# Optimization experiments

Measured on AMD Instinct MI355X. Metric: run time of the kernel, lower is better.

The kernel has to match this reference:

```python
import jax, jax.numpy as jnp
import numpy as np

B, S, D, H = 2, 2048, 1024, 16
DEPTH = D // H


def setup_inputs() -> dict:
    key = jax.random.key(0)
    ks = jax.random.split(key, 12)
    sc = 1.0 / np.sqrt(D)
    inp = {
        "q": jax.random.normal(ks[0], (B, S, D), jnp.float32),
        "v": jax.random.normal(ks[1], (B, S, D), jnp.float32),
        "k": jax.random.normal(ks[2], (B, S, D), jnp.float32),
        "mask": jnp.zeros((B, 1, S, S), jnp.float32),
        "wq_w": jax.random.normal(ks[3], (D, D), jnp.float32) * sc,
        "wq_b": jnp.zeros((D,), jnp.float32),
        "wk_w": jax.random.normal(ks[4], (D, D), jnp.float32) * sc,
        "wk_b": jnp.zeros((D,), jnp.float32),
        "wv_w": jax.random.normal(ks[5], (D, D), jnp.float32) * sc,
        "wv_b": jnp.zeros((D,), jnp.float32),
        "dense_w": jax.random.normal(ks[6], (D, D), jnp.float32) * sc,
        "dense_b": jnp.zeros((D,), jnp.float32),
    }
    return inp


def _split_heads(x):
    # (B, S, D) -> (B, H, S, depth)
    b, s, _ = x.shape
    return x.reshape(b, s, H, DEPTH).transpose(0, 2, 1, 3)


def reference(q, v, k, mask, wq_w, wq_b, wk_w, wk_b, wv_w, wv_b, dense_w, dense_b):
    batch_size = q.shape[0]
    # torch nn.Linear: x @ W.T + b
    qh = _split_heads(q @ wq_w.T + wq_b)
    kh = _split_heads(k @ wk_w.T + wk_b)
    vh = _split_heads(v @ wv_w.T + wv_b)
    temperature = jnp.asarray(DEPTH ** 0.5, qh.dtype)
    # scores: (B, H, Sq, Sk)
    qk = jnp.einsum("bhqd,bhkd->bhqk", qh, kh) / temperature
    qk = qk + mask * (-1e9)
    attention_weights = jax.nn.softmax(qk, axis=-1)
    out = jnp.einsum("bhqk,bhkd->bhqd", attention_weights, vh)
    out = out.transpose(0, 2, 1, 3).reshape(batch_size, -1, D)
    out = out @ dense_w.T + dense_b
    return (out, attention_weights)
```

## Files before the change

### kernel.cpp

```cpp
#include <hip/hip_runtime.h>
#include <cstdint>
#include <cstddef>

#define Bv   2
#define Sv   2048
#define Dv   1024
#define Hv   16
#define DEP  64
#define BHv  32
#define MROWS 4096

typedef float    f32x4 __attribute__((ext_vector_type(4)));
typedef float    f32x2 __attribute__((ext_vector_type(2)));
typedef _Float16 f16x8 __attribute__((ext_vector_type(8)));
typedef _Float16 f16x4 __attribute__((ext_vector_type(4)));
typedef _Float16 f16x2 __attribute__((ext_vector_type(2)));

__global__ __launch_bounds__(256) void convert_kernel(
    const float* __restrict__ q,  const float* __restrict__ k,  const float* __restrict__ v,
    const float* __restrict__ wq, const float* __restrict__ wk, const float* __restrict__ wv,
    const float* __restrict__ wd, const float* __restrict__ mask,
    _Float16* __restrict__ qx, _Float16* __restrict__ kx, _Float16* __restrict__ vx,
    _Float16* __restrict__ wqh, _Float16* __restrict__ wkh, _Float16* __restrict__ wvh,
    _Float16* __restrict__ wdh, _Float16* __restrict__ mlog)
{
    const size_t t = (size_t)blockIdx.x * 256 + threadIdx.x;
    {
        f32x4 m = *(const f32x4*)(mask + t * 4);
        const float sc = -1.442695040888963e9f;
        f32x4 s = { m.x * sc, m.y * sc, m.z * sc, m.w * sc };
        *(f16x4*)(mlog + t * 4) = __builtin_convertvector(s, f16x4);
    }
    {
        f32x2 a = *(const f32x2*)(q + t * 2);
        *(f16x2*)(qx + t * 2) = __builtin_convertvector(a, f16x2);
        f32x2 b = *(const f32x2*)(k + t * 2);
        *(f16x2*)(kx + t * 2) = __builtin_convertvector(b, f16x2);
        f32x2 c = *(const f32x2*)(v + t * 2);
        *(f16x2*)(vx + t * 2) = __builtin_convertvector(c, f16x2);
    }
    if (t < 524288) {
        f32x2 a = *(const f32x2*)(wq + t * 2);
        *(f16x2*)(wqh + t * 2) = __builtin_convertvector(a, f16x2);
        f32x2 b = *(const f32x2*)(wk + t * 2);
        *(f16x2*)(wkh + t * 2) = __builtin_convertvector(b, f16x2);
        f32x2 c = *(const f32x2*)(wv + t * 2);
        *(f16x2*)(wvh + t * 2) = __builtin_convertvector(c, f16x2);
        f32x2 d = *(const f32x2*)(wd + t * 2);
        *(f16x2*)(wdh + t * 2) = __builtin_convertvector(d, f16x2);
    }
}

#define LDT 40

__device__ __forceinline__ void gemm_core_128(
    const _Float16* __restrict__ A, const _Float16* __restrict__ W,
    int m0, int n0, _Float16* sA, _Float16* sW, f32x4 acc[4][4])
{
    const int tid  = threadIdx.x;
    const int lane = tid & 63, wave = tid >> 6;
    const int wm = (wave & 1) * 64, wn = (wave >> 1) * 64;
    const int fl = lane & 15, fq = lane >> 4;

    for (int k0 = 0; k0 < 1024; k0 += 32) {
        __syncthreads();
#pragma unroll
        for (int i = 0; i < 2; i++) {
            int s = tid + i * 256;
            int row = s >> 2, ch = s & 3;
            *(f16x8*)&sA[row * LDT + ch * 8] =
                *(const f16x8*)(A + (size_t)(m0 + row) * 1024 + k0 + ch * 8);
            *(f16x8*)&sW[row * LDT + ch * 8] =
                *(const f16x8*)(W + (size_t)(n0 + row) * 1024 + k0 + ch * 8);
        }
        __syncthreads();
        f16x8 af[4], wf[4];
#pragma unroll
        for (int i = 0; i < 4; i++)
            af[i] = *(const f16x8*)&sA[(wm + i * 16 + fl) * LDT + fq * 8];
#pragma unroll
        for (int j = 0; j < 4; j++)
            wf[j] = *(const f16x8*)&sW[(wn + j * 16 + fl) * LDT + fq * 8];
#pragma unroll
        for (int i = 0; i < 4; i++)
#pragma unroll
            for (int j = 0; j < 4; j++)
                acc[i][j] = __builtin_amdgcn_mfma_f32_16x16x32_f16(
                    af[i], wf[j], acc[i][j], 0, 0, 0);
    }
}

__global__ __launch_bounds__(256) void proj_gemm(
    const _Float16* __restrict__ qx, const _Float16* __restrict__ kx, const _Float16* __restrict__ vx,
    const _Float16* __restrict__ wqh, const _Float16* __restrict__ wkh, const _Float16* __restrict__ wvh,
    const float* __restrict__ bq, const float* __restrict__ bk, const float* __restrict__ bv,
    _Float16* __restrict__ qh, _Float16* __restrict__ kh, _Float16* __restrict__ vt)
{
    const _Float16* A; const _Float16* W; const float* bias; _Float16* outp; int transp;
    if (blockIdx.z == 0)      { A = qx; W = wqh; bias = bq; outp = qh; transp = 0; }
    else if (blockIdx.z == 1) { A = kx; W = wkh; bias = bk; outp = kh; transp = 0; }
    else                      { A = vx; W = wvh; bias = bv; outp = vt; transp = 1; }

    __shared__ _Float16 sA[128 * LDT];
    __shared__ _Float16 sW[128 * LDT];
    const int m0 = blockIdx.y * 128, n0 = blockIdx.x * 128;
    const int lane = threadIdx.x & 63, wave = threadIdx.x >> 6;
    const int wm = (wave & 1) * 64, wn = (wave >> 1) * 64;
    const int fl = lane & 15, fq = lane >> 4;

    f32x4 acc[4][4] = {};
    gemm_core_128(A, W, m0, n0, sA, sW, acc);

#pragma unroll
    for (int i = 0; i < 4; i++) {
#pragma unroll
        for (int j = 0; j < 4; j++) {
            int n = n0 + wn + j * 16 + fl;
            float bvv = bias[n];
            int h = n >> 6, d = n & 63;
#pragma unroll
            for (int r = 0; r < 4; r++) {
                int m = m0 + wm + i * 16 + fq * 4 + r;
                int b = m >> 11, s = m & 2047;
                float val = acc[i][j][r] + bvv;
                size_t addr;
                if (!transp) addr = (((size_t)(b * 16 + h) * 2048 + s) << 6) + d;
                else         addr = (((size_t)(b * 16 + h) * 64 + d) << 11) + s;
                outp[addr] = (_Float16)val;
            }
        }
    }
}

__global__ __launch_bounds__(256) void dense_gemm(
    const _Float16* __restrict__ A, const _Float16* __restrict__ W,
    const float* __restrict__ bias, float* __restrict__ outp)
{
    __shared__ _Float16 sA[128 * LDT];
    __shared__ _Float16 sW[128 * LDT];
    const int m0 = blockIdx.y * 128, n0 = blockIdx.x * 128;
    const int lane = threadIdx.x & 63, wave = threadIdx.x >> 6;
    const int wm = (wave & 1) * 64, wn = (wave >> 1) * 64;
    const int fl = lane & 15, fq = lane >> 4;

    f32x4 acc[4][4] = {};
    gemm_core_128(A, W, m0, n0, sA, sW, acc);

#pragma unroll
    for (int i = 0; i < 4; i++) {
#pragma unroll
        for (int j = 0; j < 4; j++) {
            int n = n0 + wn + j * 16 + fl;
            float bvv = bias[n];
#pragma unroll
            for (int r = 0; r < 4; r++) {
                int m = m0 + wm + i * 16 + fq * 4 + r;
                outp[(size_t)m * 1024 + n] = acc[i][j][r] + bvv;
            }
        }
    }
}

#define LK 72
#define LV 136
#define LP 136

__global__ __launch_bounds__(256) void attn_kernel(
    const _Float16* __restrict__ qh, const _Float16* __restrict__ kh,
    const _Float16* __restrict__ vt, const _Float16* __restrict__ mlog,
    float* __restrict__ attw, _Float16* __restrict__ ob)
{
    __shared__ _Float16 sK[128 * LK];
    __shared__ _Float16 sV[64 * LV];
    __shared__ _Float16 sP[4][16 * LP];

    const int tid = threadIdx.x, lane = tid & 63, wave = tid >> 6;
    const int bh = blockIdx.y;
    const int b  = bh >> 4;
    const int q0 = blockIdx.x * 64 + wave * 16;
    const int fl = lane & 15, fq = lane >> 4;
    const _Float16* Kb = kh + (size_t)bh * 2048 * 64;
    const _Float16* Vb = vt + (size_t)bh * 64 * 2048;
    const _Float16* Mb = mlog + ((size_t)b * 2048 + q0) * 2048;
    const float SC = 0.18033688011112042f;

    f16x8 qf[2];
    {
        const _Float16* Qb = qh + ((size_t)bh * 2048 + q0 + fl) * 64;
        qf[0] = *(const f16x8*)(Qb + fq * 8);
        qf[1] = *(const f16x8*)(Qb + 32 + fq * 8);
    }

    float lacc[4] = {0.f, 0.f, 0.f, 0.f};

    for (int kc = 0; kc < 16; kc++) {
        __syncthreads();
#pragma unroll
        for (int i = 0; i < 4; i++) {
            int s = tid + i * 256;
            int row = s >> 3, ch = s & 7;
            *(f16x8*)&sK[row * LK + ch * 8] =
                *(const f16x8*)(Kb + (size_t)(kc * 128 + row) * 64 + ch * 8);
        }
        __syncthreads();
#pragma unroll
        for (int nt = 0; nt < 8; nt++) {
            f16x8 kf0 = *(const f16x8*)&sK[(nt * 16 + fl) * LK + fq * 8];
            f16x8 kf1 = *(const f16x8*)&sK[(nt * 16 + fl) * LK + 32 + fq * 8];
            f32x4 sacc = {};
            sacc = __builtin_amdgcn_mfma_f32_16x16x32_f16(qf[0], kf0, sacc, 0, 0, 0);
            sacc = __builtin_amdgcn_mfma_f32_16x16x32_f16(qf[1], kf1, sacc, 0, 0, 0);
            int key = kc * 128 + nt * 16 + fl;
#pragma unroll
            for (int r = 0; r < 4; r++) {
                float mval = (float)Mb[(size_t)(fq * 4 + r) * 2048 + key];
                lacc[r] += exp2f(sacc[r] * SC + mval);
            }
        }
    }
#pragma unroll
    for (int r = 0; r < 4; r++) {
        float x = lacc[r];
        x += __shfl_xor(x, 1);
        x += __shfl_xor(x, 2);
        x += __shfl_xor(x, 4);
        x += __shfl_xor(x, 8);
        lacc[r] = 1.0f / x;
    }

    f32x4 oacc[4] = {};

    for (int kc = 0; kc < 16; kc++) {
        __syncthreads();
#pragma unroll
        for (int i = 0; i < 4; i++) {
            int s = tid + i * 256;
            int row = s >> 3, ch = s & 7;
            *(f16x8*)&sK[row * LK + ch * 8] =
                *(const f16x8*)(Kb + (size_t)(kc * 128 + row) * 64 + ch * 8);
        }
#pragma unroll
        for (int i = 0; i < 4; i++) {
            int s = tid + i * 256;
            int row = s >> 4, ch = s & 15;
            *(f16x8*)&sV[row * LV + ch * 8] =
                *(const f16x8*)(Vb + (size_t)row * 2048 + kc * 128 + ch * 8);
        }
        __syncthreads();
#pragma unroll
        for (int nt = 0; nt < 8; nt++) {
            f16x8 kf0 = *(const f16x8*)&sK[(nt * 16 + fl) * LK + fq * 8];
            f16x8 kf1 = *(const f16x8*)&sK[(nt * 16 + fl) * LK + 32 + fq * 8];
            f32x4 sacc = {};
            sacc = __builtin_amdgcn_mfma_f32_16x16x32_f16(qf[0], kf0, sacc, 0, 0, 0);
            sacc = __builtin_amdgcn_mfma_f32_16x16x32_f16(qf[1], kf1, sacc, 0, 0, 0);
            int key = kc * 128 + nt * 16 + fl;
#pragma unroll
            for (int r = 0; r < 4; r++) {
                float mval = (float)Mb[(size_t)(fq * 4 + r) * 2048 + key];
                float p = exp2f(sacc[r] * SC + mval) * lacc[r];
                attw[((size_t)bh * 2048 + q0 + fq * 4 + r) * 2048 + key] = p;
                sP[wave][(fq * 4 + r) * LP + nt * 16 + fl] = (_Float16)p;
            }
        }
        __syncthreads();
#pragma unroll
        for (int km = 0; km < 4; km++) {
            f16x8 pf = *(const f16x8*)&sP[wave][fl * LP + km * 32 + fq * 8];
#pragma unroll
            for (int dt = 0; dt < 4; dt++) {
                f16x8 vf = *(const f16x8*)&sV[(dt * 16 + fl) * LV + km * 32 + fq * 8];
                oacc[dt] = __builtin_amdgcn_mfma_f32_16x16x32_f16(pf, vf, oacc[dt], 0, 0, 0);
            }
        }
    }

    const int h = bh & 15;
#pragma unroll
    for (int dt = 0; dt < 4; dt++) {
#pragma unroll
        for (int r = 0; r < 4; r++) {
            int qrow = q0 + fq * 4 + r;
            ob[((size_t)(b * 2048 + qrow)) * 1024 + h * 64 + dt * 16 + fl] =
                (_Float16)oacc[dt][r];
        }
    }
}

extern "C" void kernel_launch(void* const* d_in, const int* in_sizes, int n_in,
                              void* d_out, int out_size, void* d_ws, size_t ws_size,
                              hipStream_t stream)
{
    const float* q       = (const float*)d_in[0];
    const float* v       = (const float*)d_in[1];
    const float* k       = (const float*)d_in[2];
    const float* mask    = (const float*)d_in[3];
    const float* wq_w    = (const float*)d_in[4];
    const float* wq_b    = (const float*)d_in[5];
    const float* wk_w    = (const float*)d_in[6];
    const float* wk_b    = (const float*)d_in[7];
    const float* wv_w    = (const float*)d_in[8];
    const float* wv_b    = (const float*)d_in[9];
    const float* dense_w = (const float*)d_in[10];
    const float* dense_b = (const float*)d_in[11];

    char* ws = (char*)d_ws;
    _Float16* qx   = (_Float16*)(ws + 0);
    _Float16* kx   = (_Float16*)(ws + 8388608);
    _Float16* vx   = (_Float16*)(ws + 16777216);
    _Float16* wqh  = (_Float16*)(ws + 25165824);
    _Float16* wkh  = (_Float16*)(ws + 27262976);
    _Float16* wvh  = (_Float16*)(ws + 29360128);
    _Float16* wdh  = (_Float16*)(ws + 31457280);
    _Float16* qhp  = (_Float16*)(ws + 33554432);
    _Float16* khp  = (_Float16*)(ws + 41943040);
    _Float16* vtp  = (_Float16*)(ws + 50331648);
    _Float16* obp  = (_Float16*)(ws + 58720256);
    _Float16* mlog = (_Float16*)(ws + 67108864);

    float* outp = (float*)d_out;
    float* attw = outp + (size_t)4194304;

    convert_kernel<<<8192, 256, 0, stream>>>(q, k, v, wq_w, wk_w, wv_w, dense_w,
                                             mask, qx, kx, vx, wqh, wkh, wvh, wdh, mlog);
    proj_gemm<<<dim3(8, 32, 3), 256, 0, stream>>>(qx, kx, vx, wqh, wkh, wvh,
                                                  wq_b, wk_b, wv_b, qhp, khp, vtp);
    attn_kernel<<<dim3(32, 32), 256, 0, stream>>>(qhp, khp, vtp, mlog, attw, obp);
    dense_gemm<<<dim3(8, 32), 256, 0, stream>>>(obp, wdh, dense_b, outp);
}
```

Baseline: 1.063 ms.

## Compute scores once per 16-row block, split keys across waves

The attention kernel is restructured so each block handles 16 query rows, and its four waves each take a quarter of the key range. Exponentiated scores are computed once and kept unnormalized in fp16 shared memory, instead of being recomputed in a second pass after the row sum is known. Row sums and partial P·V outputs are then reduced across waves through shared memory. The attention-weight output is written as coalesced vector stores, but those weights now come from fp16-rounded values, and K and V are read directly from global memory rather than staged in shared memory. The grid grows fourfold, and the large shared buffer (about 66 KB) may limit occupancy.

Measured after the change: 1.003 ms. -5.7%, faster.

```diff
diff --git a/kernel.cpp b/kernel.cpp
--- a/kernel.cpp
+++ b/kernel.cpp
@@ -161,129 +161,108 @@
     }
 }
 
-#define LK 72
-#define LV 136
-#define LP 136
+#define LPB 2056
 
 __global__ __launch_bounds__(256) void attn_kernel(
     const _Float16* __restrict__ qh, const _Float16* __restrict__ kh,
     const _Float16* __restrict__ vt, const _Float16* __restrict__ mlog,
     float* __restrict__ attw, _Float16* __restrict__ ob)
 {
-    __shared__ _Float16 sK[128 * LK];
-    __shared__ _Float16 sV[64 * LV];
-    __shared__ _Float16 sP[4][16 * LP];
-
-    const int tid = threadIdx.x, lane = tid & 63, wave = tid >> 6;
-    const int bh = blockIdx.y;
-    const int b  = bh >> 4;
-    const int q0 = blockIdx.x * 64 + wave * 16;
-    const int fl = lane & 15, fq = lane >> 4;
-    const _Float16* Kb = kh + (size_t)bh * 2048 * 64;
-    const _Float16* Vb = vt + (size_t)bh * 64 * 2048;
-    const _Float16* Mb = mlog + ((size_t)b * 2048 + q0) * 2048;
+    __shared__ _Float16 pbuf[16 * LPB];
+    __shared__ float    lred[4][16];
+
+    const int tid  = threadIdx.x, lane = tid & 63, wave = tid >> 6;
+    const int fl   = lane & 15,   fq   = lane >> 4;
+    const int bh   = blockIdx.y,  b    = bh >> 4, h = bh & 15;
+    const int q0   = blockIdx.x * 16;
+    const int kwb  = wave * 512;
     const float SC = 0.18033688011112042f;
 
-    f16x8 qf[2];
-    {
-        const _Float16* Qb = qh + ((size_t)bh * 2048 + q0 + fl) * 64;
-        qf[0] = *(const f16x8*)(Qb + fq * 8);
-        qf[1] = *(const f16x8*)(Qb + 32 + fq * 8);
-    }
-
-    float lacc[4] = {0.f, 0.f, 0.f, 0.f};
-
-    for (int kc = 0; kc < 16; kc++) {
-        __syncthreads();
-#pragma unroll
-        for (int i = 0; i < 4; i++) {
-            int s = tid + i * 256;
-            int row = s >> 3, ch = s & 7;
-            *(f16x8*)&sK[row * LK + ch * 8] =
-                *(const f16x8*)(Kb + (size_t)(kc * 128 + row) * 64 + ch * 8);
-        }
-        __syncthreads();
-#pragma unroll
-        for (int nt = 0; nt < 8; nt++) {
-            f16x8 kf0 = *(const f16x8*)&sK[(nt * 16 + fl) * LK + fq * 8];
-            f16x8 kf1 = *(const f16x8*)&sK[(nt * 16 + fl) * LK + 32 + fq * 8];
-            f32x4 sacc = {};
-            sacc = __builtin_amdgcn_mfma_f32_16x16x32_f16(qf[0], kf0, sacc, 0, 0, 0);
-            sacc = __builtin_amdgcn_mfma_f32_16x16x32_f16(qf[1], kf1, sacc, 0, 0, 0);
-            int key = kc * 128 + nt * 16 + fl;
-#pragma unroll
-            for (int r = 0; r < 4; r++) {
-                float mval = (float)Mb[(size_t)(fq * 4 + r) * 2048 + key];
-                lacc[r] += exp2f(sacc[r] * SC + mval);
-            }
-        }
-    }
-#pragma unroll
-    for (int r = 0; r < 4; r++) {
-        float x = lacc[r];
-        x += __shfl_xor(x, 1);
-        x += __shfl_xor(x, 2);
-        x += __shfl_xor(x, 4);
-        x += __shfl_xor(x, 8);
-        lacc[r] = 1.0f / x;
+    const _Float16* Kb   = kh   + (size_t)bh * 2048 * 64;
+    const _Float16* Vb   = vt   + (size_t)bh * 64 * 2048;
+    const _Float16* Mrow = mlog + ((size_t)b * 2048 + q0 + fl) * 2048 + kwb;
+
+    f16x8 qf0, qf1;
+    {
+        const _Float16* Qp = qh + ((size_t)bh * 2048 + q0 + fl) * 64;
+        qf0 = *(const f16x8*)(Qp + fq * 8);
+        qf1 = *(const f16x8*)(Qp + 32 + fq * 8);
+    }
+
+    float lacc = 0.f;
+#pragma unroll
+    for (int t = 0; t < 32; t++) {
+        const int key0 = kwb + t * 16;
+        const _Float16* Kp = Kb + (size_t)(key0 + fl) * 64 + fq * 8;
+        f16x8 kf0 = *(const f16x8*)Kp;
+        f16x8 kf1 = *(const f16x8*)(Kp + 32);
+        f16x4 mv  = *(const f16x4*)(Mrow + t * 16 + fq * 4);
+        f32x4 sacc = {};
+        sacc = __builtin_amdgcn_mfma_f32_16x16x32_f16(kf0, qf0, sacc, 0, 0, 0);
+        sacc = __builtin_amdgcn_mfma_f32_16x16x32_f16(kf1, qf1, sacc, 0, 0, 0);
+        f16x4 ph;
+#pragma unroll
+        for (int r = 0; r < 4; r++) {
+            float p = exp2f(sacc[r] * SC + (float)mv[r]);
+            lacc += p;
+            ph[r] = (_Float16)p;
+        }
+        *(f16x4*)&pbuf[(size_t)fl * LPB + key0 + fq * 4] = ph;
+    }
+    lacc += __shfl_xor(lacc, 16);
+    lacc += __shfl_xor(lacc, 32);
+    if (fq == 0) lred[wave][fl] = lacc;
+
+    __syncthreads();
+
+    {
+        float* aw = attw + ((size_t)bh * 2048 + q0) * 2048 + kwb + lane * 8;
+#pragma unroll
+        for (int row = 0; row < 16; row++) {
+            float ls = lred[0][row] + lred[1][row] + lred[2][row] + lred[3][row];
+            float rl = 1.0f / ls;
+            f16x8 pv = *(const f16x8*)&pbuf[row * LPB + kwb + lane * 8];
+            f32x4 o0 = { (float)pv[0] * rl, (float)pv[1] * rl,
+                         (float)pv[2] * rl, (float)pv[3] * rl };
+            f32x4 o1 = { (float)pv[4] * rl, (float)pv[5] * rl,
+                         (float)pv[6] * rl, (float)pv[7] * rl };
+            *(f32x4*)(aw + (size_t)row * 2048)     = o0;
+            *(f32x4*)(aw + (size_t)row * 2048 + 4) = o1;
+        }
     }
 
     f32x4 oacc[4] = {};
-
-    for (int kc = 0; kc < 16; kc++) {
-        __syncthreads();
-#pragma unroll
-        for (int i = 0; i < 4; i++) {
-            int s = tid + i * 256;
-            int row = s >> 3, ch = s & 7;
-            *(f16x8*)&sK[row * LK + ch * 8] =
-                *(const f16x8*)(Kb + (size_t)(kc * 128 + row) * 64 + ch * 8);
-        }
-#pragma unroll
-        for (int i = 0; i < 4; i++) {
-            int s = tid + i * 256;
-            int row = s >> 4, ch = s & 15;
-            *(f16x8*)&sV[row * LV + ch * 8] =
-                *(const f16x8*)(Vb + (size_t)row * 2048 + kc * 128 + ch * 8);
-        }
-        __syncthreads();
-#pragma unroll
-        for (int nt = 0; nt < 8; nt++) {
-            f16x8 kf0 = *(const f16x8*)&sK[(nt * 16 + fl) * LK + fq * 8];
-            f16x8 kf1 = *(const f16x8*)&sK[(nt * 16 + fl) * LK + 32 + fq * 8];
-            f32x4 sacc = {};
-            sacc = __builtin_amdgcn_mfma_f32_16x16x32_f16(qf[0], kf0, sacc, 0, 0, 0);
-            sacc = __builtin_amdgcn_mfma_f32_16x16x32_f16(qf[1], kf1, sacc, 0, 0, 0);
-            int key = kc * 128 + nt * 16 + fl;
-#pragma unroll
-            for (int r = 0; r < 4; r++) {
-                float mval = (float)Mb[(size_t)(fq * 4 + r) * 2048 + key];
-                float p = exp2f(sacc[r] * SC + mval) * lacc[r];
-                attw[((size_t)bh * 2048 + q0 + fq * 4 + r) * 2048 + key] = p;
-                sP[wave][(fq * 4 + r) * LP + nt * 16 + fl] = (_Float16)p;
-            }
-        }
-        __syncthreads();
-#pragma unroll
-        for (int km = 0; km < 4; km++) {
-            f16x8 pf = *(const f16x8*)&sP[wave][fl * LP + km * 32 + fq * 8];
-#pragma unroll
-            for (int dt = 0; dt < 4; dt++) {
-                f16x8 vf = *(const f16x8*)&sV[(dt * 16 + fl) * LV + km * 32 + fq * 8];
-                oacc[dt] = __builtin_amdgcn_mfma_f32_16x16x32_f16(pf, vf, oacc[dt], 0, 0, 0);
-            }
-        }
-    }
-
-    const int h = bh & 15;
-#pragma unroll
-    for (int dt = 0; dt < 4; dt++) {
-#pragma unroll
-        for (int r = 0; r < 4; r++) {
-            int qrow = q0 + fq * 4 + r;
-            ob[((size_t)(b * 2048 + qrow)) * 1024 + h * 64 + dt * 16 + fl] =
-                (_Float16)oacc[dt][r];
-        }
+#pragma unroll
+    for (int kk = 0; kk < 16; kk++) {
+        f16x8 pf = *(const f16x8*)&pbuf[(size_t)fl * LPB + kwb + kk * 32 + fq * 8];
+#pragma unroll
+        for (int dt = 0; dt < 4; dt++) {
+            f16x8 vf = *(const f16x8*)(Vb + (size_t)(dt * 16 + fl) * 2048
+                                       + kwb + kk * 32 + fq * 8);
+            oacc[dt] = __builtin_amdgcn_mfma_f32_16x16x32_f16(pf, vf, oacc[dt], 0, 0, 0);
+        }
+    }
+
+    __syncthreads();
+    float* ored = (float*)pbuf;
+#pragma unroll
+    for (int dt = 0; dt < 4; dt++)
+#pragma unroll
+        for (int r = 0; r < 4; r++)
+            ored[(wave * 16 + fq * 4 + r) * 68 + dt * 16 + fl] = oacc[dt][r];
+    __syncthreads();
+
+    {
+        const int row = tid >> 4, d4 = (tid & 15) * 4;
+        f32x4 s = {};
+#pragma unroll
+        for (int w = 0; w < 4; w++)
+            s += *(const f32x4*)&ored[(w * 16 + row) * 68 + d4];
+        float ls = lred[0][row] + lred[1][row] + lred[2][row] + lred[3][row];
+        float rl = 1.0f / ls;
+        f16x4 hv = { (_Float16)(s[0] * rl), (_Float16)(s[1] * rl),
+                     (_Float16)(s[2] * rl), (_Float16)(s[3] * rl) };
+        *(f16x4*)(ob + ((size_t)(b * 2048 + q0 + row)) * 1024 + h * 64 + d4) = hv;
     }
 }
 
@@ -325,6 +304,6 @@
                                              mask, qx, kx, vx, wqh, wkh, wvh, wdh, mlog);
     proj_gemm<<<dim3(8, 32, 3), 256, 0, stream>>>(qx, kx, vx, wqh, wkh, wvh,
                                                   wq_b, wk_b, wv_b, qhp, khp, vtp);
-    attn_kernel<<<dim3(32, 32), 256, 0, stream>>>(qhp, khp, vtp, mlog, attw, obp);
+    attn_kernel<<<dim3(128, 32), 256, 0, stream>>>(qhp, khp, vtp, mlog, attw, obp);
     dense_gemm<<<dim3(8, 32), 256, 0, stream>>>(obp, wdh, dense_b, outp);
 }
```
